# Kernel tuning notes

Measured on AMD Instinct MI355X. Metric: run time of the kernel, lower is better.

## Reference

```python
import jax, jax.numpy as jnp
import numpy as np

NH = 8       # attention_maps
DK = 256     # key_dimension
DV = 256     # value_dimension
KS = 3       # kernel_size
PAD = (KS - 1) // 2


def _conv(x, w, b, stride, pad):
    y = jax.lax.conv_general_dilated(
        x, w, (stride, stride), [(pad, pad), (pad, pad)],
        dimension_numbers=('NCHW', 'OIHW', 'NCHW'))
    return y + b[None, :, None, None]


def _rel_to_abs(x):
    # x: (B, M, L, 2L-1) -> (B, M, L, L) via the skewing/padding trick
    B, M, L, _ = x.shape
    x = jnp.pad(x, ((0, 0), (0, 0), (0, 0), (0, 1)))          # (B,M,L,2L)
    x = x.reshape(B, M, 2 * L * L)
    x = jnp.pad(x, ((0, 0), (0, 0), (0, L - 1)))
    x = x.reshape(B, M, L + 1, 2 * L - 1)
    return x[:, :, :L, L - 1:]


def _rel_logits_1d(q, kr, H, W, nh, axis):
    # q: (B, nh, H, W, dkh); kr: (2W-1, dkh)
    B = q.shape[0]
    rl = jnp.einsum('bhxyd,md->bhxym', q, kr)                 # (B,nh,H,W,2W-1)
    rl = rl.reshape(B, nh * H, W, 2 * W - 1)
    rl = _rel_to_abs(rl).reshape(B, nh, H, W, W)
    rl = jnp.broadcast_to(rl[:, :, :, None], (B, nh, H, H, W, W))
    if axis == 'x':
        rl = jnp.transpose(rl, (0, 1, 2, 4, 3, 5))
    else:
        # faithful to original torch code (incl. its no-op transpose bug):
        # transpose(4,5) then transpose(3,5) == permutation (0,1,2,4,5,3)
        rl = jnp.transpose(rl, (0, 1, 2, 4, 5, 3))
    return rl.reshape(B, nh, H * W, H * W)


def setup_inputs() -> dict:
    key = jax.random.key(0)
    ks = jax.random.split(key, 10)
    B, Cin, H, W = 4, 128, 32, 32
    Cout = 512
    dkh = DK // NH
    sc = 0.05
    return {
        'x': jax.random.normal(ks[0], (B, Cin, H, W), jnp.float32),
        'conv_w': jax.random.normal(ks[1], (Cout - DV, Cin, KS, KS), jnp.float32) * sc,
        'conv_b': jax.random.normal(ks[2], (Cout - DV,), jnp.float32) * sc,
        'qkv_w': jax.random.normal(ks[3], (2 * DK + DV, Cin, KS, KS), jnp.float32) * sc,
        'qkv_b': jax.random.normal(ks[4], (2 * DK + DV,), jnp.float32) * sc,
        'att_w': jax.random.normal(ks[5], (DV, DV, 1, 1), jnp.float32) * sc,
        'att_b': jax.random.normal(ks[6], (DV,), jnp.float32) * sc,
        'kr_x': jax.random.normal(ks[7], (2 * W - 1, dkh), jnp.float32),
        'kr_y': jax.random.normal(ks[8], (2 * H - 1, dkh), jnp.float32),
    }


def reference(x, conv_w, conv_b, qkv_w, qkv_b, att_w, att_b, kr_x, kr_y):
    B = x.shape[0]
    conv_out = _conv(x, conv_w, conv_b, 1, PAD)               # (B, Cout-DV, H, W)
    H, W = conv_out.shape[2], conv_out.shape[3]
    dkh, dvh = DK // NH, DV // NH

    qkv = _conv(x, qkv_w, qkv_b, 1, PAD)                      # (B, 2DK+DV, H, W)
    q, k, v = jnp.split(qkv, [DK, 2 * DK], axis=1)
    q = q.reshape(B, NH, dkh, H, W) * (dkh ** -0.5)
    k = k.reshape(B, NH, dkh, H, W)
    v = v.reshape(B, NH, dvh, H, W)

    fq = q.reshape(B, NH, dkh, H * W)
    fk = k.reshape(B, NH, dkh, H * W)
    fv = v.reshape(B, NH, dvh, H * W)

    logits = jnp.einsum('bhdi,bhdj->bhij', fq, fk)            # (B,NH,HW,HW)

    # relative logits (scaled q, matching torch which scales before this)
    q_t = jnp.transpose(q, (0, 1, 3, 4, 2))                   # (B,NH,H,W,dkh)
    rel_x = _rel_logits_1d(q_t, kr_x, H, W, NH, 'x')
    rel_y = _rel_logits_1d(jnp.transpose(q_t, (0, 1, 3, 2, 4)), kr_y, W, H, NH, 'y')
    logits = logits + rel_y + rel_x

    weights = jax.nn.softmax(logits, axis=-1)
    att = jnp.einsum('bhij,bhdj->bhid', weights, fv)          # (B,NH,HW,dvh)
    # faithful raw reshape as in torch (no transpose before reshape)
    att = att.reshape(B, NH, dvh, H, W).reshape(B, DV, H, W)
    att = _conv(att, att_w, att_b, 1, 0)
    return jnp.concatenate([conv_out, att], axis=1)
```

## Files before the change

kernel.cpp:

```cpp
#include <hip/hip_runtime.h>
#include <hip/hip_bf16.h>
#include <math.h>

#define BN 4
#define CIN 128
#define HH 32
#define WW 32
#define HWP 1024
#define NHEAD 8

typedef __attribute__((ext_vector_type(8))) short s8v;
typedef __attribute__((ext_vector_type(4))) float f32x4;

__global__ __launch_bounds__(256) void prep_all(
    const float* __restrict__ x,
    const float* __restrict__ conv_w, const float* __restrict__ qkv_w,
    const float* __restrict__ att_w,
    const float* __restrict__ kr_x, const float* __restrict__ kr_y,
    __hip_bfloat16* __restrict__ xT, __hip_bfloat16* __restrict__ Wb,
    __hip_bfloat16* __restrict__ Wab, __hip_bfloat16* __restrict__ krb)
{
    const int bid = blockIdx.x;
    const int tid = threadIdx.x;

    if (bid < 128) {
        __shared__ __hip_bfloat16 Ws[8 * 1152];
        const int co0 = bid * 8;
        const float* src = (co0 < 256) ? (conv_w + (size_t)co0 * 1152)
                                       : (qkv_w + (size_t)(co0 - 256) * 1152);
#pragma unroll
        for (int pass = 0; pass < 36; ++pass) {
            int idx = pass * 256 + tid;
            float v = src[idx];
            int col = idx / 1152;
            int r = idx - col * 1152;
            int ci = r / 9;
            int kk = r - ci * 9;
            Ws[col * 1152 + kk * 128 + ci] = __float2bfloat16(v);
        }
        __syncthreads();
        const unsigned* Lu = (const unsigned*)Ws;
        unsigned* Ou = (unsigned*)(Wb + (size_t)co0 * 1152);
#pragma unroll
        for (int pass = 0; pass < 18; ++pass)
            Ou[pass * 256 + tid] = Lu[pass * 256 + tid];
    } else if (bid < 264) {
        __shared__ float xs[CIN][33];
        int rel = bid - 128;
        int yy = rel >> 2;
        int b = rel & 3;
        const bool inner = (yy >= 1 && yy <= 32);
        if (inner) {
            for (int idx = tid; idx < CIN * 32; idx += 256) {
                int ci = idx >> 5, xx = idx & 31;
                xs[ci][xx] = x[((size_t)(b * CIN + ci) * HH + (yy - 1)) * WW + xx];
            }
        }
        __syncthreads();
        for (int idx = tid; idx < 34 * 128; idx += 256) {
            int xx = idx >> 7, ci = idx & 127;
            float v = 0.f;
            if (inner && xx >= 1 && xx <= 32) v = xs[ci][xx - 1];
            xT[((size_t)(b * 34 + yy) * 34 + xx) * 128 + ci] = __float2bfloat16(v);
        }
    } else if (bid < 328) {
        int g = ((bid - 264) * 256 + tid) * 4;
        float4 v = *(const float4*)(att_w + g);
        Wab[g + 0] = __float2bfloat16(v.x);
        Wab[g + 1] = __float2bfloat16(v.y);
        Wab[g + 2] = __float2bfloat16(v.z);
        Wab[g + 3] = __float2bfloat16(v.w);
    } else {
        for (int idx = tid; idx < 2 * 64 * 32; idx += 256) {
            int axis = idx >> 11;
            int col = (idx >> 5) & 63;
            int d = idx & 31;
            float v = 0.f;
            if (col < 63) v = axis ? kr_y[col * 32 + d] : kr_x[col * 32 + d];
            krb[idx] = __float2bfloat16(v);
        }
    }
}

__global__ __launch_bounds__(256) void conv_gemm(
    const __hip_bfloat16* __restrict__ Wb, const __hip_bfloat16* __restrict__ xT,
    const float* __restrict__ conv_b, const float* __restrict__ qkv_b,
    float* __restrict__ out,
    __hip_bfloat16* __restrict__ qbf, __hip_bfloat16* __restrict__ kbf,
    __hip_bfloat16* __restrict__ vtb)
{
    __shared__ __align__(16) __hip_bfloat16 As[128 * 128];
    __shared__ __align__(16) __hip_bfloat16 Bs[64 * 128];

    const int tid = threadIdx.x;
    const int wv = tid >> 6;
    const int lane = tid & 63;
    const int n16 = lane & 15;
    const int quad = lane >> 4;
    const int bid = blockIdx.x;
    const int ph = bid & 1;
    const int b = (bid >> 1) & 3;
    const int yt = (bid >> 3) & 7;
    const int ct = bid >> 6;
    const int co0 = ct * 128;
    const int pixBase = yt * 128 + ph * 64;
    const int row0 = pixBase >> 5;
    const int mh = wv >> 1, nh = wv & 1;
    const int rbase = tid >> 4;
    const int hh = tid & 15;
    const int swz = (hh ^ rbase) * 8;
    const __hip_bfloat16* aGbase = Wb + (size_t)(co0 + rbase) * 1152 + hh * 8;

    f32x4 acc[4][2];
#pragma unroll
    for (int i = 0; i < 4; ++i)
#pragma unroll
        for (int j = 0; j < 2; ++j) acc[i][j] = (f32x4){0.f, 0.f, 0.f, 0.f};

    s8v ra[8], rb2[4];
    auto load_tile = [&](int kk, s8v* la, s8v* lb) {
        const int ky = kk / 3, kx = kk - ky * 3;
#pragma unroll
        for (int i = 0; i < 8; ++i)
            la[i] = *reinterpret_cast<const s8v*>(aGbase + (size_t)(16 * i) * 1152 + kk * 128);
#pragma unroll
        for (int i = 0; i < 4; ++i) {
            int p = rbase + 16 * i;
            lb[i] = *reinterpret_cast<const s8v*>(
                xT + ((size_t)(b * 34 + row0 + (p >> 5) + ky) * 34 + (p & 31) + kx) * 128 + hh * 8);
        }
    };

    load_tile(0, ra, rb2);

    for (int s = 0; s < 9; ++s) {
        __syncthreads();
#pragma unroll
        for (int i = 0; i < 8; ++i)
            *reinterpret_cast<s8v*>(&As[(rbase + 16 * i) * 128 + swz]) = ra[i];
#pragma unroll
        for (int i = 0; i < 4; ++i)
            *reinterpret_cast<s8v*>(&Bs[(rbase + 16 * i) * 128 + swz]) = rb2[i];
        __syncthreads();
        if (s < 8) load_tile(s + 1, ra, rb2);

#pragma unroll
        for (int ksub = 0; ksub < 4; ++ksub) {
            const int chunk = ((ksub * 4 + quad) ^ n16) * 8;
            s8v af[4], bfr[2];
#pragma unroll
            for (int mt = 0; mt < 4; ++mt)
                af[mt] = *reinterpret_cast<const s8v*>(&As[(mh * 64 + mt * 16 + n16) * 128 + chunk]);
#pragma unroll
            for (int nt = 0; nt < 2; ++nt)
                bfr[nt] = *reinterpret_cast<const s8v*>(&Bs[(nh * 32 + nt * 16 + n16) * 128 + chunk]);
#pragma unroll
            for (int mt = 0; mt < 4; ++mt)
#pragma unroll
                for (int nt = 0; nt < 2; ++nt)
                    acc[mt][nt] = __builtin_amdgcn_mfma_f32_16x16x32_bf16(af[mt], bfr[nt], acc[mt][nt], 0, 0, 0);
        }
    }

    const int coBase = co0 + mh * 64;
    const int pixW = pixBase + nh * 32;
    const int seg = coBase >> 8;

    if (seg == 0) {
#pragma unroll
        for (int mt = 0; mt < 4; ++mt)
#pragma unroll
            for (int r = 0; r < 4; ++r) {
                int co = coBase + mt * 16 + quad * 4 + r;
                float bias = conv_b[co];
                float* op = out + (size_t)(b * 512 + co) * HWP + pixW;
#pragma unroll
                for (int nt = 0; nt < 2; ++nt)
                    op[nt * 16 + n16] = acc[mt][nt][r] + bias;
            }
    } else if (seg == 1) {
        const float scale = 0.17677669529663687f;
#pragma unroll
        for (int mt = 0; mt < 4; ++mt)
#pragma unroll
            for (int r = 0; r < 4; ++r) {
                int c2 = coBase - 256 + mt * 16 + quad * 4 + r;
                float bias = qkv_b[c2];
                int h = c2 >> 5, d = c2 & 31;
                int bh = b * NHEAD + h;
#pragma unroll
                for (int nt = 0; nt < 2; ++nt) {
                    int pix = pixW + nt * 16 + n16;
                    qbf[((size_t)bh * HWP + pix) * 32 + d] =
                        __float2bfloat16((acc[mt][nt][r] + bias) * scale);
                }
            }
    } else if (seg == 2) {
#pragma unroll
        for (int mt = 0; mt < 4; ++mt)
#pragma unroll
            for (int r = 0; r < 4; ++r) {
                int c2 = coBase - 512 + mt * 16 + quad * 4 + r;
                float bias = qkv_b[c2 + 256];
                int h = c2 >> 5, d = c2 & 31;
                int bh = b * NHEAD + h;
#pragma unroll
                for (int nt = 0; nt < 2; ++nt) {
                    int pix = pixW + nt * 16 + n16;
                    kbf[((size_t)bh * HWP + pix) * 32 + d] =
                        __float2bfloat16(acc[mt][nt][r] + bias);
                }
            }
    } else {
#pragma unroll
        for (int mt = 0; mt < 4; ++mt)
#pragma unroll
            for (int r = 0; r < 4; ++r) {
                int c2 = coBase - 768 + mt * 16 + quad * 4 + r;
                float bias = qkv_b[c2 + 512];
                int h = c2 >> 5, d = c2 & 31;
                int bh = b * NHEAD + h;
                __hip_bfloat16* vp = vtb + ((size_t)bh * 32 + d) * HWP + pixW;
#pragma unroll
                for (int nt = 0; nt < 2; ++nt)
                    vp[nt * 16 + n16] = __float2bfloat16(acc[mt][nt][r] + bias);
            }
    }
}

__global__ __launch_bounds__(256) void attn_kernel(
    const __hip_bfloat16* __restrict__ qbf, const __hip_bfloat16* __restrict__ kbf,
    const __hip_bfloat16* __restrict__ vtb, const __hip_bfloat16* __restrict__ krb,
    __hip_bfloat16* __restrict__ attc)
{
    __shared__ __align__(16) float QrX[4][16][68];
    __shared__ __align__(16) float QrY[4][16][68];
    __shared__ __align__(16) __hip_bfloat16 Pb[4][16][40];

    const int tid = threadIdx.x;
    const int wv = tid >> 6;
    const int lane = tid & 63;
    const int n16 = lane & 15;
    const int quad = lane >> 4;
    const int bh = blockIdx.x;
    const int i0 = (blockIdx.y * 4 + wv) * 16;
    const int xi0 = i0 & 31;
    const int yi0 = i0 >> 5;

    s8v aq = *reinterpret_cast<const s8v*>(
        qbf + ((size_t)bh * HWP + i0 + n16) * 32 + quad * 8);
    s8v aqT = *reinterpret_cast<const s8v*>(
        qbf + ((size_t)bh * HWP + (xi0 + n16) * 32 + yi0) * 32 + quad * 8);

#pragma unroll
    for (int t = 0; t < 4; ++t) {
        s8v bx = *reinterpret_cast<const s8v*>(krb + ((size_t)(t * 16 + n16)) * 32 + quad * 8);
        s8v by = *reinterpret_cast<const s8v*>(krb + ((size_t)(64 + t * 16 + n16)) * 32 + quad * 8);
        f32x4 cx = {0.f, 0.f, 0.f, 0.f}, cy = {0.f, 0.f, 0.f, 0.f};
        cx = __builtin_amdgcn_mfma_f32_16x16x32_bf16(aq, bx, cx, 0, 0, 0);
        cy = __builtin_amdgcn_mfma_f32_16x16x32_bf16(aqT, by, cy, 0, 0, 0);
#pragma unroll
        for (int r = 0; r < 4; ++r) {
            QrX[wv][quad * 4 + r][t * 16 + n16] = cx[r];
            QrY[wv][quad * 4 + r][t * 16 + n16] = cy[r];
        }
    }

    float rx0[4], rx1[4];
    int rybase[4];
#pragma unroll
    for (int r = 0; r < 4; ++r) {
        int xi = xi0 + quad * 4 + r;
        rx0[r] = QrX[wv][quad * 4 + r][n16 + 31 - xi];
        rx1[r] = QrX[wv][quad * 4 + r][n16 + 47 - xi];
        rybase[r] = 31 - xi;
    }

    float lsum[4] = {0.f, 0.f, 0.f, 0.f};
    f32x4 O0 = {0.f, 0.f, 0.f, 0.f}, O1 = {0.f, 0.f, 0.f, 0.f};

    const __hip_bfloat16* kbase = kbf + (size_t)bh * HWP * 32;
    const __hip_bfloat16* vbase = vtb + (size_t)bh * 32 * HWP;

    s8v bk0 = *reinterpret_cast<const s8v*>(kbase + ((size_t)n16 * 32 + quad * 8));
    s8v bk1 = *reinterpret_cast<const s8v*>(kbase + ((size_t)(16 + n16) * 32 + quad * 8));
    s8v bv0 = *reinterpret_cast<const s8v*>(vbase + ((size_t)n16 * HWP + quad * 8));
    s8v bv1 = *reinterpret_cast<const s8v*>(vbase + ((size_t)(n16 + 16) * HWP + quad * 8));

    for (int jt = 0; jt < 32; ++jt) {
        s8v cbk0 = bk0, cbk1 = bk1, cbv0 = bv0, cbv1 = bv1;
        if (jt < 31) {
            const int jn = (jt + 1) * 32;
            bk0 = *reinterpret_cast<const s8v*>(kbase + ((size_t)(jn + n16) * 32 + quad * 8));
            bk1 = *reinterpret_cast<const s8v*>(kbase + ((size_t)(jn + 16 + n16) * 32 + quad * 8));
            bv0 = *reinterpret_cast<const s8v*>(vbase + ((size_t)n16 * HWP + jn + quad * 8));
            bv1 = *reinterpret_cast<const s8v*>(vbase + ((size_t)(n16 + 16) * HWP + jn + quad * 8));
        }

        f32x4 s0 = {0.f, 0.f, 0.f, 0.f}, s1 = {0.f, 0.f, 0.f, 0.f};
        s0 = __builtin_amdgcn_mfma_f32_16x16x32_bf16(aq, cbk0, s0, 0, 0, 0);
        s1 = __builtin_amdgcn_mfma_f32_16x16x32_bf16(aq, cbk1, s1, 0, 0, 0);

#pragma unroll
        for (int r = 0; r < 4; ++r) {
            float ryv = QrY[wv][quad * 4 + r][jt + rybase[r]];
            float p0 = __expf(s0[r] + rx0[r] + ryv);
            float p1 = __expf(s1[r] + rx1[r] + ryv);
            lsum[r] += p0 + p1;
            Pb[wv][quad * 4 + r][n16]      = __float2bfloat16(p0);
            Pb[wv][quad * 4 + r][n16 + 16] = __float2bfloat16(p1);
        }
        s8v pA = *reinterpret_cast<const s8v*>(&Pb[wv][n16][quad * 8]);
        O0 = __builtin_amdgcn_mfma_f32_16x16x32_bf16(pA, cbv0, O0, 0, 0, 0);
        O1 = __builtin_amdgcn_mfma_f32_16x16x32_bf16(pA, cbv1, O1, 0, 0, 0);
    }

    const int b = bh >> 3, h = bh & 7;
#pragma unroll
    for (int r = 0; r < 4; ++r) {
        float l = lsum[r];
        l += __shfl_xor(l, 1);
        l += __shfl_xor(l, 2);
        l += __shfl_xor(l, 4);
        l += __shfl_xor(l, 8);
        float inv = 1.0f / l;
        int i = i0 + quad * 4 + r;
        int yi = i >> 5, xi = i & 31;
        __hip_bfloat16* op = attc + ((size_t)(b * 256 + h * 32 + yi) * 32 + xi) * 32;
        op[n16] = __float2bfloat16(O0[r] * inv);
        op[n16 + 16] = __float2bfloat16(O1[r] * inv);
    }
}

__global__ __launch_bounds__(256) void conv1x1_gemm(
    const __hip_bfloat16* __restrict__ Wab, const __hip_bfloat16* __restrict__ attc,
    const float* __restrict__ att_b, float* __restrict__ out)
{
    __shared__ __align__(16) __hip_bfloat16 Ls[64][264];

    const int tid = threadIdx.x;
    const int wv = tid >> 6;
    const int lane = tid & 63;
    const int n16 = lane & 15;
    const int quad = lane >> 4;
    const int o0 = blockIdx.x * 64;
    const int p0 = blockIdx.y * 64;
    const int b = blockIdx.z;
    const int oW = o0 + (wv >> 1) * 32;
    const int pL = (wv & 1) * 32;

#pragma unroll
    for (int pass = 0; pass < 8; ++pass) {
        int ch = pass * 32 + (tid >> 3);
        int pg = (tid & 7) * 8;
        s8v v = *reinterpret_cast<const s8v*>(
            attc + ((size_t)(b * 256 + ch) * HWP) + p0 + pg);
#pragma unroll
        for (int j = 0; j < 8; ++j)
            Ls[pg + j][ch] = ((const __hip_bfloat16*)&v)[j];
    }
    __syncthreads();

    f32x4 acc[2][2];
#pragma unroll
    for (int i = 0; i < 2; ++i)
#pragma unroll
        for (int j = 0; j < 2; ++j) acc[i][j] = (f32x4){0.f, 0.f, 0.f, 0.f};

#pragma unroll
    for (int ks = 0; ks < 8; ++ks) {
        const int c0 = ks * 32 + quad * 8;
        s8v a0 = *reinterpret_cast<const s8v*>(Wab + (size_t)(oW + n16) * 256 + c0);
        s8v a1 = *reinterpret_cast<const s8v*>(Wab + (size_t)(oW + 16 + n16) * 256 + c0);
        s8v b0 = *reinterpret_cast<const s8v*>(&Ls[pL + n16][c0]);
        s8v b1 = *reinterpret_cast<const s8v*>(&Ls[pL + 16 + n16][c0]);
        acc[0][0] = __builtin_amdgcn_mfma_f32_16x16x32_bf16(a0, b0, acc[0][0], 0, 0, 0);
        acc[0][1] = __builtin_amdgcn_mfma_f32_16x16x32_bf16(a0, b1, acc[0][1], 0, 0, 0);
        acc[1][0] = __builtin_amdgcn_mfma_f32_16x16x32_bf16(a1, b0, acc[1][0], 0, 0, 0);
        acc[1][1] = __builtin_amdgcn_mfma_f32_16x16x32_bf16(a1, b1, acc[1][1], 0, 0, 0);
    }

#pragma unroll
    for (int mt = 0; mt < 2; ++mt)
#pragma unroll
        for (int r = 0; r < 4; ++r) {
            int o = oW + mt * 16 + quad * 4 + r;
            float bias = att_b[o];
            float* op = out + ((size_t)(b * 512 + 256 + o)) * HWP;
#pragma unroll
            for (int nt = 0; nt < 2; ++nt)
                op[p0 + pL + nt * 16 + n16] = acc[mt][nt][r] + bias;
        }
}

extern "C" void kernel_launch(void* const* d_in, const int* in_sizes, int n_in,
                              void* d_out, int out_size, void* d_ws, size_t ws_size,
                              hipStream_t stream) {
    const float* x      = (const float*)d_in[0];
    const float* conv_w = (const float*)d_in[1];
    const float* conv_b = (const float*)d_in[2];
    const float* qkv_w  = (const float*)d_in[3];
    const float* qkv_b  = (const float*)d_in[4];
    const float* att_w  = (const float*)d_in[5];
    const float* att_b  = (const float*)d_in[6];
    const float* kr_x   = (const float*)d_in[7];
    const float* kr_y   = (const float*)d_in[8];
    float* out = (float*)d_out;

    char* base = (char*)d_ws;
    const size_t MB = 1u << 20;
    __hip_bfloat16* qbf  = (__hip_bfloat16*)(base + 0 * MB);
    __hip_bfloat16* kbf  = (__hip_bfloat16*)(base + 2 * MB);
    __hip_bfloat16* vtb  = (__hip_bfloat16*)(base + 4 * MB);
    __hip_bfloat16* xT   = (__hip_bfloat16*)(base + 6 * MB);
    __hip_bfloat16* Wb   = (__hip_bfloat16*)(base + 8 * MB);
    __hip_bfloat16* attc = (__hip_bfloat16*)(base + 11 * MB);
    __hip_bfloat16* Wab  = (__hip_bfloat16*)(base + 13 * MB);
    __hip_bfloat16* krb  = (__hip_bfloat16*)(base + 14 * MB);

    prep_all<<<dim3(329), 256, 0, stream>>>(
        x, conv_w, qkv_w, att_w, kr_x, kr_y, xT, Wb, Wab, krb);
    conv_gemm<<<dim3(512), 256, 0, stream>>>(
        Wb, xT, conv_b, qkv_b, out, qbf, kbf, vtb);
    attn_kernel<<<dim3(32, 16), 256, 0, stream>>>(qbf, kbf, vtb, krb, attc);
    conv1x1_gemm<<<dim3(4, 16, 4), 256, 0, stream>>>(Wab, attc, att_b, out);
}
```

Before: 134.0 us.

## Load conv GEMM weight fragments directly from global memory, bypassing LDS

The conv GEMM kernel no longer stages the weight (A) tile through shared memory. Each wave now loads its MFMA A fragments straight from global memory, prefetching one k-substep ahead in registers. This halves LDS usage and removes the LDS write/read traffic for A, which could raise occupancy. The cost is that the two wave pairs sharing the same mh rows both fetch those weights, and the global loads are less coalesced because they fall on the critical path of each k-substep.

Measured after the change: 155.1 us. 1.16x slower.

```diff
diff --git a/kernel.cpp b/kernel.cpp
--- a/kernel.cpp
+++ b/kernel.cpp
@@ -89,7 +89,6 @@
     __hip_bfloat16* __restrict__ qbf, __hip_bfloat16* __restrict__ kbf,
     __hip_bfloat16* __restrict__ vtb)
 {
-    __shared__ __align__(16) __hip_bfloat16 As[128 * 128];
     __shared__ __align__(16) __hip_bfloat16 Bs[64 * 128];
 
     const int tid = threadIdx.x;
@@ -109,7 +108,6 @@
     const int rbase = tid >> 4;
     const int hh = tid & 15;
     const int swz = (hh ^ rbase) * 8;
-    const __hip_bfloat16* aGbase = Wb + (size_t)(co0 + rbase) * 1152 + hh * 8;
 
     f32x4 acc[4][2];
 #pragma unroll
@@ -117,12 +115,14 @@
 #pragma unroll
         for (int j = 0; j < 2; ++j) acc[i][j] = (f32x4){0.f, 0.f, 0.f, 0.f};
 
-    s8v ra[8], rb2[4];
-    auto load_tile = [&](int kk, s8v* la, s8v* lb) {
+    const __hip_bfloat16* aRow[4];
+#pragma unroll
+    for (int mt = 0; mt < 4; ++mt)
+        aRow[mt] = Wb + (size_t)(co0 + mh * 64 + mt * 16 + n16) * 1152 + quad * 8;
+
+    s8v rb2[4];
+    auto load_tileB = [&](int kk, s8v* lb) {
         const int ky = kk / 3, kx = kk - ky * 3;
-#pragma unroll
-        for (int i = 0; i < 8; ++i)
-            la[i] = *reinterpret_cast<const s8v*>(aGbase + (size_t)(16 * i) * 1152 + kk * 128);
 #pragma unroll
         for (int i = 0; i < 4; ++i) {
             int p = rbase + 16 * i;
@@ -131,29 +131,37 @@
         }
     };
 
-    load_tile(0, ra, rb2);
+    s8v afn[4];
+    auto loadA = [&](int t, s8v* a) {
+#pragma unroll
+        for (int mt = 0; mt < 4; ++mt)
+            a[mt] = *reinterpret_cast<const s8v*>(aRow[mt] + t * 32);
+    };
+
+    load_tileB(0, rb2);
+    loadA(0, afn);
 
     for (int s = 0; s < 9; ++s) {
         __syncthreads();
-#pragma unroll
-        for (int i = 0; i < 8; ++i)
-            *reinterpret_cast<s8v*>(&As[(rbase + 16 * i) * 128 + swz]) = ra[i];
 #pragma unroll
         for (int i = 0; i < 4; ++i)
             *reinterpret_cast<s8v*>(&Bs[(rbase + 16 * i) * 128 + swz]) = rb2[i];
         __syncthreads();
-        if (s < 8) load_tile(s + 1, ra, rb2);
+        if (s < 8) load_tileB(s + 1, rb2);
 
 #pragma unroll
         for (int ksub = 0; ksub < 4; ++ksub) {
-            const int chunk = ((ksub * 4 + quad) ^ n16) * 8;
-            s8v af[4], bfr[2];
-#pragma unroll
-            for (int mt = 0; mt < 4; ++mt)
-                af[mt] = *reinterpret_cast<const s8v*>(&As[(mh * 64 + mt * 16 + n16) * 128 + chunk]);
+            s8v af[4];
+#pragma unroll
+            for (int mt = 0; mt < 4; ++mt) af[mt] = afn[mt];
+            const int tnext = s * 4 + ksub + 1;
+            if (tnext < 36) loadA(tnext, afn);
+
+            s8v bfr[2];
 #pragma unroll
             for (int nt = 0; nt < 2; ++nt)
-                bfr[nt] = *reinterpret_cast<const s8v*>(&Bs[(nh * 32 + nt * 16 + n16) * 128 + chunk]);
+                bfr[nt] = *reinterpret_cast<const s8v*>(
+                    &Bs[(nh * 32 + nt * 16 + n16) * 128 + ((ksub * 4 + quad) ^ n16) * 8]);
 #pragma unroll
             for (int mt = 0; mt < 4; ++mt)
 #pragma unroll
```
